# Performance work log

Hardware: AMD Instinct MI355X
Metric: run time of the kernel (lower is better)

The kernel has to match this reference:

```python
import jax, jax.numpy as jnp
import numpy as np

# Model constants (match init_kwargs)
B, V, NUM_NODES, NUM_RELS = 32, 20, 4000, 400
EMB, HID, L, N, E, OUT = 128, 128, 3, 32000, 256000, 128
DECAY = 0.03
EPS = 0.0  # self_attn eps, not trained


def setup_inputs() -> dict:
    key = jax.random.key(0)
    ks = jax.random.split(key, 20)
    s = 0.02
    return {
        "node_ids": jax.random.randint(ks[0], (N,), 0, NUM_NODES),
        "rel_ids": jax.random.randint(ks[1], (E,), 0, NUM_RELS),
        "edge_index": jax.random.randint(ks[2], (2, E), 0, N),
        "batch": jnp.sort(jax.random.randint(ks[3], (N,), 0, B)),
        "visit_node": jax.random.uniform(ks[4], (B, V, NUM_NODES), dtype=jnp.float32),
        "ehr_nodes": jax.random.uniform(ks[5], (B, NUM_NODES), dtype=jnp.float32),
        "node_emb": jax.random.normal(ks[6], (NUM_NODES, EMB), dtype=jnp.float32) * s,
        "rel_emb": jax.random.normal(ks[7], (NUM_RELS, EMB), dtype=jnp.float32) * s,
        "lin_w": jax.random.normal(ks[8], (HID, EMB), dtype=jnp.float32) * s,
        "lin_b": jnp.zeros((HID,), jnp.float32),
        "alpha_w": jax.random.normal(ks[9], (L, NUM_NODES, NUM_NODES), dtype=jnp.float32) * 0.002,
        "alpha_b": jnp.zeros((L, NUM_NODES), jnp.float32),
        "beta_w": jax.random.normal(ks[10], (L, 1, NUM_NODES), dtype=jnp.float32) * s,
        "beta_b": jnp.zeros((L, 1), jnp.float32),
        "wr_w": jax.random.normal(ks[11], (L, 1, HID), dtype=jnp.float32) * s,
        "wr_b": jnp.zeros((L, 1), jnp.float32),
        "nn_w": jax.random.normal(ks[12], (L, HID, HID), dtype=jnp.float32) * s,
        "nn_b": jnp.zeros((L, HID), jnp.float32),
        "mlp_w": jax.random.normal(ks[13], (OUT, 2 * HID), dtype=jnp.float32) * s,
        "mlp_b": jnp.zeros((OUT,), jnp.float32),
    }


def reference(node_ids, rel_ids, edge_index, batch, visit_node, ehr_nodes,
              node_emb, rel_emb, lin_w, lin_b, alpha_w, alpha_b, beta_w, beta_b,
              wr_w, wr_b, nn_w, nn_b, mlp_w, mlp_b):
    # visit decay weights lambda_j: (1, V, 1)
    lambda_j = jnp.exp(DECAY * (V - jnp.arange(V, dtype=jnp.float32))).reshape(1, V, 1)

    x = node_emb[node_ids] @ lin_w.T + lin_b          # (N, HID)
    edge_attr = rel_emb[rel_ids] @ lin_w.T + lin_b    # (E, HID)
    src, dst = edge_index[0], edge_index[1]
    nid_src = node_ids[src]
    b_src = batch[src]

    for l in range(L):
        # alpha: softmax over visit dim, (B, V, NUM_NODES)
        alpha = jax.nn.softmax(
            jnp.einsum('bvn,mn->bvm', visit_node, alpha_w[l]) + alpha_b[l], axis=1)
        # beta: (B, V, 1) with visit decay
        beta = jnp.tanh(
            jnp.einsum('bvn,on->bvo', visit_node, beta_w[l]) + beta_b[l]) * lambda_j
        attn = jnp.sum(alpha * beta, axis=1)          # (B, NUM_NODES)
        e_attn = attn[b_src, nid_src][:, None]        # (E, 1) per-edge attention

        # BiAttentionGNNConv message: relu(x_j * attn + W_R(edge_attr) * edge_attr)
        w_rel = edge_attr @ wr_w[l].T + wr_b[l]       # (E, 1)
        msg = jax.nn.relu(x[src] * e_attn + w_rel * edge_attr)
        agg = jax.ops.segment_sum(msg, dst, num_segments=N)  # scatter-add aggregate
        out = agg + (1.0 + EPS) * x                   # eps residual
        x = jax.nn.relu(out @ nn_w[l].T + nn_b[l])    # conv.nn Linear + outer relu

    # graph-level patient embedding: global mean pool over batch
    counts = jnp.maximum(
        jax.ops.segment_sum(jnp.ones((N, 1), x.dtype), batch, num_segments=B), 1.0)
    x_graph = jax.ops.segment_sum(x, batch, num_segments=B) / counts  # (B, HID)

    # node-level patient embedding: ehr multihot average of node embeddings
    x_node = (ehr_nodes @ node_emb) / jnp.sum(ehr_nodes, axis=1, keepdims=True)
    x_node = x_node @ lin_w.T + lin_b                 # (B, HID)

    logits = jnp.concatenate([x_graph, x_node], axis=1) @ mlp_w.T + mlp_b
    return logits
```

## Files before the change

### kernel.cpp

```cpp
#include <hip/hip_runtime.h>

namespace {

constexpr int kNodes = 4000;
constexpr int kRels  = 400;
constexpr int kB     = 32;
constexpr int kV     = 20;
constexpr int kN     = 32000;
constexpr int kE     = 256000;
constexpr int kH     = 128;
constexpr int kL     = 3;
constexpr int kMPad  = 4096;
constexpr int kKPad  = 4096;
constexpr int kBV    = kB * kV;
constexpr int kNB    = 32;
constexpr int kChunk = kE / kNB;
constexpr int kHalf  = 16000;

typedef __attribute__((ext_vector_type(8))) short bf16x8;
typedef __attribute__((ext_vector_type(4))) float f32x4;

__device__ inline unsigned short f2bf(float f){
  unsigned int u = __float_as_uint(f);
  u += 0x7FFFu + ((u >> 16) & 1u);
  return (unsigned short)(u >> 16);
}

__device__ inline void gload_lds16(const unsigned short* g, unsigned short* l){
  __builtin_amdgcn_global_load_lds(
      (const __attribute__((address_space(1))) unsigned int*)(g),
      (__attribute__((address_space(3))) unsigned int*)(l),
      16, 0, 0);
}


__global__ void transpose_kernel(const float* __restrict__ lin_w, const float* __restrict__ nn_w,
                                 float* __restrict__ lin_wT, float* __restrict__ nn_wT){
  int m = blockIdx.x;
  const float* in = (m == 0) ? lin_w : nn_w + (size_t)(m-1)*kH*kH;
  float* out      = (m == 0) ? lin_wT : nn_wT + (size_t)(m-1)*kH*kH;
  for (int i = threadIdx.x; i < kH*kH; i += blockDim.x){
    int r = i >> 7, c = i & (kH-1);
    out[c*kH + r] = in[i];
  }
}

__global__ __launch_bounds__(128) void proj_kernel(const float* __restrict__ node_emb,
    const float* __restrict__ rel_emb, const float* __restrict__ lin_wT,
    const float* __restrict__ lin_b, float* __restrict__ emb_lin, float* __restrict__ rel_lin){
  int row = blockIdx.x;
  const float* src; float* dst;
  if (row < kNodes){ src = node_emb + (size_t)row*kH; dst = emb_lin + (size_t)row*kH; }
  else             { src = rel_emb + (size_t)(row-kNodes)*kH; dst = rel_lin + (size_t)(row-kNodes)*kH; }
  __shared__ float rs[kH];
  int h = threadIdx.x;
  rs[h] = src[h];
  __syncthreads();
  float acc = lin_b[h];
#pragma unroll 8
  for (int k = 0; k < kH; k++) acc = fmaf(rs[k], lin_wT[k*kH + h], acc);
  dst[h] = acc;
}

__global__ void gather_x0_kernel(const int* __restrict__ node_ids,
                                 const float* __restrict__ emb_lin, float* __restrict__ x){
  int idx = blockIdx.x*256 + threadIdx.x;
  if (idx < kN*kH){
    int i = idx >> 7, c = idx & (kH-1);
    x[idx] = emb_lin[(size_t)node_ids[i]*kH + c];
  }
}

__global__ __launch_bounds__(128) void relterm_kernel(const float* __restrict__ rel_lin,
    const float* __restrict__ wr_w, const float* __restrict__ wr_b, float* __restrict__ relterm){
  int l = blockIdx.x / kRels, r = blockIdx.x % kRels;
  int t = threadIdx.x;
  float rl = rel_lin[(size_t)r*kH + t];
  __shared__ float red[kH];
  red[t] = rl * wr_w[l*kH + t];
  __syncthreads();
  for (int o = 64; o > 0; o >>= 1){
    if (t < o) red[t] += red[t+o];
    __syncthreads();
  }
  float w = red[0] + wr_b[l];
  relterm[((size_t)l*kRels + r)*kH + t] = w * rl;
}


__global__ __launch_bounds__(256) void csr_hist_kernel(const int* __restrict__ dst,
    unsigned short* __restrict__ rank, unsigned int* __restrict__ hpart){
  __shared__ unsigned int hb[kHalf];
  int p = blockIdx.x;
  int base = blockIdx.y * kHalf;
  int t = threadIdx.x;
  for (int i = t; i < kHalf; i += 256) hb[i] = 0u;
  __syncthreads();
  for (int i = t; i < kChunk; i += 256){
    int e = p*kChunk + i;
    int d = dst[e];
    int rel = d - base;
    if ((unsigned)rel < (unsigned)kHalf){
      rank[e] = (unsigned short)atomicAdd(&hb[rel], 1u);
    }
  }
  __syncthreads();
  for (int i = t; i < kHalf; i += 256)
    hpart[(size_t)p*kN + base + i] = hb[i];
}

__global__ __launch_bounds__(256) void csr_col_kernel(unsigned int* __restrict__ hpart,
    int* __restrict__ deg){
  int bin = blockIdx.x*256 + threadIdx.x;
  if (bin >= kN) return;
  unsigned int s = 0;
#pragma unroll
  for (int p = 0; p < kNB; p++){
    size_t idx = (size_t)p*kN + bin;
    unsigned int v = hpart[idx];
    hpart[idx] = s;
    s += v;
  }
  deg[bin] = (int)s;
}

__global__ __launch_bounds__(256) void scanA_kernel(const int* __restrict__ deg,
    int* __restrict__ starts, int* __restrict__ bsum){
  __shared__ int buf[256];
  int gid = blockIdx.x*256 + threadIdx.x;
  int t = threadIdx.x;
  int v = (gid < kN) ? deg[gid] : 0;
  buf[t] = v;
  __syncthreads();
  for (int o = 1; o < 256; o <<= 1){
    int add = (t >= o) ? buf[t-o] : 0;
    __syncthreads();
    buf[t] += add;
    __syncthreads();
  }
  if (gid < kN) starts[gid] = buf[t] - v;
  if (t == 255) bsum[blockIdx.x] = buf[255];
}

__global__ __launch_bounds__(128) void scanB_kernel(const int* __restrict__ bsum,
    int* __restrict__ boffs, int nblk){
  __shared__ int buf[128];
  int t = threadIdx.x;
  int v = (t < nblk) ? bsum[t] : 0;
  buf[t] = v;
  __syncthreads();
  for (int o = 1; o < 128; o <<= 1){
    int add = (t >= o) ? buf[t-o] : 0;
    __syncthreads();
    buf[t] += add;
    __syncthreads();
  }
  if (t < nblk) boffs[t] = buf[t] - v;
}

__global__ __launch_bounds__(256) void scanC_kernel(int* __restrict__ starts,
    const int* __restrict__ boffs){
  int gid = blockIdx.x*256 + threadIdx.x;
  if (gid < kN) starts[gid] += boffs[blockIdx.x];
  if (gid == kN-1) starts[kN] = kE;
}

__global__ __launch_bounds__(256) void csr_place_kernel(const int* __restrict__ dst,
    const int* __restrict__ starts, const unsigned int* __restrict__ colOff,
    const unsigned short* __restrict__ rank, int* __restrict__ perm){
  int blk = blockIdx.x;
  int p = blk >> 2;
  for (int i = threadIdx.x; i < 2000; i += 256){
    int e = blk*2000 + i;
    int d = dst[e];
    int pos = starts[d] + (int)colOff[(size_t)p*kN + d] + (int)rank[e];
    perm[pos] = e;
  }
}

__global__ void ub_kernel(const int* __restrict__ batch, int* __restrict__ ub){
  int j = threadIdx.x;
  if (j > kB) return;
  int lo = 0, hi = kN;
  while (lo < hi){
    int mid = (lo + hi) >> 1;
    if (batch[mid] < j) lo = mid + 1; else hi = mid;
  }
  ub[j] = lo;
}


__global__ void cvt_visit_kernel(const float* __restrict__ visit, unsigned short* __restrict__ out){
  int i = blockIdx.x*256 + threadIdx.x;
  if (i >= kBV*(kKPad/8)) return;
  int row = i >> 9;
  int col = (i & 511) * 8;
  unsigned short r[8];
  if (col < kNodes){
    const float* p = visit + (size_t)row*kNodes + col;
    const float4 a = *reinterpret_cast<const float4*>(p);
    const float4 b = *reinterpret_cast<const float4*>(p + 4);
    r[0]=f2bf(a.x); r[1]=f2bf(a.y); r[2]=f2bf(a.z); r[3]=f2bf(a.w);
    r[4]=f2bf(b.x); r[5]=f2bf(b.y); r[6]=f2bf(b.z); r[7]=f2bf(b.w);
  } else {
    for (int q = 0; q < 8; q++) r[q] = 0;
  }
  *reinterpret_cast<uint4*>(out + (size_t)row*kKPad + col) = *reinterpret_cast<uint4*>(r);
}

__global__ void cvtW_kernel(const float* __restrict__ W, unsigned short* __restrict__ out){
  int i = blockIdx.x*256 + threadIdx.x;
  constexpr int perL = kMPad*(kKPad/8);
  if (i >= kL*perL) return;
  int l = i / perL;
  int rem = i - l*perL;
  int row = rem >> 9;
  int col = (rem & 511) * 8;
  unsigned short r[8];
  if (row < kNodes && col < kNodes){
    const float* p = W + (size_t)l*kNodes*kNodes + (size_t)row*kNodes + col;
    const float4 a = *reinterpret_cast<const float4*>(p);
    const float4 b = *reinterpret_cast<const float4*>(p + 4);
    r[0]=f2bf(a.x); r[1]=f2bf(a.y); r[2]=f2bf(a.z); r[3]=f2bf(a.w);
    r[4]=f2bf(b.x); r[5]=f2bf(b.y); r[6]=f2bf(b.z); r[7]=f2bf(b.w);
  } else {
    for (int q = 0; q < 8; q++) r[q] = 0;
  }
  *reinterpret_cast<uint4*>(out + (size_t)l*kMPad*kKPad + (size_t)row*kKPad + col)
      = *reinterpret_cast<uint4*>(r);
}

__global__ __launch_bounds__(256) void gemm_bt_bf16(const unsigned short* __restrict__ A,
    const unsigned short* __restrict__ Ball, float* __restrict__ Sbase){
  __shared__ unsigned short As[128*64];
  __shared__ unsigned short Bs[128*64];
  int wg = (blockIdx.x & 7)*120 + (blockIdx.x >> 3);
  int lz = wg / 160;
  int rem = wg - lz*160;
  int bn = rem / 5;
  int bm = rem - bn*5;
  int l = lz >> 1, z = lz & 1;
  const unsigned short* B = Ball + (size_t)l*kMPad*kKPad;
  float* C = Sbase + (size_t)lz*kBV*kMPad;
  int kBase = z * 2048;

  int t = threadIdx.x;
  int lane = t & 63, wave = t >> 6;
  int wm = (wave >> 1) * 64, wn = (wave & 1) * 64;
  int r = lane & 15, g = lane >> 4;

  int ri = lane >> 3, s = lane & 7;
  int koff = ((s ^ ri) << 3);
  const unsigned short* Ag = A + (size_t)(bm*128 + wave*32 + ri)*kKPad + kBase + koff;
  const unsigned short* Bg = B + (size_t)(bn*128 + wave*32 + ri)*kKPad + kBase + koff;
  const size_t chunkStep = (size_t)8*kKPad;

  f32x4 acc[4][4];
#pragma unroll
  for (int i = 0; i < 4; i++)
#pragma unroll
    for (int j = 0; j < 4; j++) acc[i][j] = f32x4{0.f,0.f,0.f,0.f};

  for (int k0 = 0; k0 < 2048; k0 += 64){
    __syncthreads();
#pragma unroll
    for (int c = 0; c < 4; c++){
      gload_lds16(Ag + c*chunkStep, &As[(wave*32 + c*8)*64]);
      gload_lds16(Bg + c*chunkStep, &Bs[(wave*32 + c*8)*64]);
    }
    Ag += 64; Bg += 64;
    __syncthreads();
#pragma unroll
    for (int ksub = 0; ksub < 2; ksub++){
      bf16x8 af[4], bf[4];
#pragma unroll
      for (int i = 0; i < 4; i++){
        int arow = wm + i*16 + r;
        int brow = wn + i*16 + r;
        int slot = ((ksub << 2) + g);
        af[i] = *reinterpret_cast<const bf16x8*>(&As[arow*64 + ((slot ^ (arow & 7)) << 3)]);
        bf[i] = *reinterpret_cast<const bf16x8*>(&Bs[brow*64 + ((slot ^ (brow & 7)) << 3)]);
      }
#pragma unroll
      for (int i = 0; i < 4; i++)
#pragma unroll
        for (int j = 0; j < 4; j++)
          acc[i][j] = __builtin_amdgcn_mfma_f32_16x16x32_bf16(af[i], bf[j], acc[i][j], 0, 0, 0);
    }
  }
#pragma unroll
  for (int i = 0; i < 4; i++)
#pragma unroll
    for (int j = 0; j < 4; j++){
      int row = bm*128 + wm + i*16 + g*4;
      int col = bn*128 + wn + j*16 + r;
#pragma unroll
      for (int q = 0; q < 4; q++)
        C[(size_t)(row + q)*kMPad + col] = acc[i][j][q];
    }
}

__global__ __launch_bounds__(256) void beta_all_kernel(const float* __restrict__ visit,
    const float* __restrict__ beta_w, const float* __restrict__ beta_b,
    float* __restrict__ beta){
  int wid = (blockIdx.x*256 + threadIdx.x) >> 6;
  int lane = threadIdx.x & 63;
  if (wid >= kL*kBV) return;
  int l = wid / kBV, bv = wid - l*kBV;
  const float* row = visit + (size_t)bv*kNodes;
  const float* bw = beta_w + (size_t)l*kNodes;
  float s = 0.f;
  for (int k = lane; k < kNodes; k += 64) s = fmaf(row[k], bw[k], s);
#pragma unroll
  for (int o = 32; o > 0; o >>= 1) s += __shfl_down(s, o);
  if (lane == 0){
    int v = bv % kV;
    float lam = __expf(0.03f * (float)(kV - v));
    beta[wid] = tanhf(s + beta_b[l]) * lam;
  }
}

__global__ __launch_bounds__(256) void attn_kernel(const float* __restrict__ S,
    const float* __restrict__ beta, float* __restrict__ attn){
  int idx = blockIdx.x*256 + threadIdx.x;
  if (idx >= kL*kB*kNodes) return;
  int l = idx / (kB*kNodes);
  int rem = idx - l*(kB*kNodes);
  int b = rem / kNodes;
  int m = rem - b*kNodes;
  const float* S0 = S + (size_t)(l*2)*kBV*kMPad + (size_t)b*kV*kMPad + m;
  const float* S1 = S0 + (size_t)kBV*kMPad;
  float vals[kV];
  float mx = -1e30f;
#pragma unroll
  for (int v = 0; v < kV; v++){
    float s = S0[(size_t)v*kMPad] + S1[(size_t)v*kMPad];
    vals[v] = s; mx = fmaxf(mx, s);
  }
  float se = 0.f, ws = 0.f;
  const float* bp = beta + l*kBV + b*kV;
#pragma unroll
  for (int v = 0; v < kV; v++){ float e = __expf(vals[v] - mx); se += e; ws = fmaf(e, bp[v], ws); }
  attn[idx] = ws / se;
}

__global__ void attn_gather_kernel(const int* __restrict__ batch,
    const int* __restrict__ node_ids, const float* __restrict__ attn,
    float* __restrict__ att_n){
  int idx = blockIdx.x*256 + threadIdx.x;
  if (idx >= kL*kN) return;
  int l = idx / kN, n = idx - l*kN;
  att_n[idx] = attn[(size_t)l*kB*kNodes + (size_t)batch[n]*kNodes + node_ids[n]];
}


__global__ __launch_bounds__(256) void agg_kernel(const int* __restrict__ starts,
    const int* __restrict__ perm, const int* __restrict__ src, const int* __restrict__ rel_ids,
    const float* __restrict__ att_n_l, const float* __restrict__ relterm_l,
    const float* __restrict__ x, float* __restrict__ agg){
  int wid = (blockIdx.x*256 + threadIdx.x) >> 6;
  int lane = threadIdx.x & 63;
  if (wid >= kN) return;
  int p0 = starts[wid], p1 = starts[wid+1];
  int c = lane*2;
  float a0 = 0.f, a1 = 0.f;
  for (int p = p0; p < p1; p++){
    int e = perm[p];
    int s = src[e];
    float at = att_n_l[s];
    float2 xv = *reinterpret_cast<const float2*>(&x[(size_t)s*kH + c]);
    float2 rt = *reinterpret_cast<const float2*>(&relterm_l[(size_t)rel_ids[e]*kH + c]);
    float m0 = fmaf(xv.x, at, rt.x); m0 = m0 > 0.f ? m0 : 0.f;
    float m1 = fmaf(xv.y, at, rt.y); m1 = m1 > 0.f ? m1 : 0.f;
    a0 += m0; a1 += m1;
  }
  *reinterpret_cast<float2*>(&agg[(size_t)wid*kH + c]) = float2{a0, a1};
}

__global__ __launch_bounds__(256) void nn_kernel(const float* __restrict__ agg,
    float* __restrict__ x, const float* __restrict__ nn_wT_l, const float* __restrict__ nn_b_l){
  __shared__ float rows[8][kH];
  int rb = blockIdx.x * 8;
  int t = threadIdx.x;
#pragma unroll
  for (int i = 0; i < 4; i++){
    int idx = t + i*256;
    int rr = idx >> 7, cc = idx & (kH-1);
    size_t gi = (size_t)(rb + rr)*kH + cc;
    rows[rr][cc] = agg[gi] + x[gi];
  }
  __syncthreads();
  int cc = t & (kH-1);
  int r0 = (t >> 7) * 4;
  float acc0 = 0.f, acc1 = 0.f, acc2 = 0.f, acc3 = 0.f;
#pragma unroll 8
  for (int k = 0; k < kH; k++){
    float w = nn_wT_l[k*kH + cc];
    acc0 = fmaf(rows[r0+0][k], w, acc0);
    acc1 = fmaf(rows[r0+1][k], w, acc1);
    acc2 = fmaf(rows[r0+2][k], w, acc2);
    acc3 = fmaf(rows[r0+3][k], w, acc3);
  }
  float b = nn_b_l[cc];
  x[(size_t)(rb+r0+0)*kH + cc] = fmaxf(acc0 + b, 0.f);
  x[(size_t)(rb+r0+1)*kH + cc] = fmaxf(acc1 + b, 0.f);
  x[(size_t)(rb+r0+2)*kH + cc] = fmaxf(acc2 + b, 0.f);
  x[(size_t)(rb+r0+3)*kH + cc] = fmaxf(acc3 + b, 0.f);
}


__global__ __launch_bounds__(128) void pool_part_kernel(const float* __restrict__ x,
    const int* __restrict__ ub, float* __restrict__ pp){
  int s = blockIdx.x, b = blockIdx.y, c = threadIdx.x;
  int lo = ub[b], len = ub[b+1] - lo;
  int i0 = lo + (int)(((long long)len * s) >> 3);
  int i1 = lo + (int)(((long long)len * (s+1)) >> 3);
  float acc = 0.f;
  for (int i = i0; i < i1; i++) acc += x[(size_t)i*kH + c];
  pp[(size_t)(b*8 + s)*kH + c] = acc;
}

__global__ __launch_bounds__(128) void xnode1_kernel(const float* __restrict__ ehr,
    const float* __restrict__ node_emb, float* __restrict__ pn, float* __restrict__ ps){
  int s = blockIdx.x, b = blockIdx.y, c = threadIdx.x;
  int n0 = s * (kNodes/8), n1 = n0 + (kNodes/8);
  float acc = 0.f, es = 0.f;
  for (int n = n0; n < n1; n++){
    float e = ehr[(size_t)b*kNodes + n];
    es += e;
    acc = fmaf(e, node_emb[(size_t)n*kH + c], acc);
  }
  pn[(size_t)(b*8 + s)*kH + c] = acc;
  if (c == 0) ps[b*8 + s] = es;
}

__global__ __launch_bounds__(128) void readout_kernel(const float* __restrict__ pp,
    const int* __restrict__ ub, const float* __restrict__ pn, const float* __restrict__ ps,
    const float* __restrict__ lin_wT, const float* __restrict__ lin_b,
    const float* __restrict__ mlp_w, const float* __restrict__ mlp_b,
    float* __restrict__ out){
  int b = blockIdx.x, h = threadIdx.x;
  __shared__ float v[2*kH];
  __shared__ float ts[kH];
  float s = 0.f;
#pragma unroll
  for (int q = 0; q < 8; q++) s += pp[(size_t)(b*8 + q)*kH + h];
  int len = ub[b+1] - ub[b]; if (len < 1) len = 1;
  v[h] = s / (float)len;
  float acc = 0.f, es = 0.f;
#pragma unroll
  for (int q = 0; q < 8; q++){
    acc += pn[(size_t)(b*8 + q)*kH + h];
    es  += ps[b*8 + q];
  }
  ts[h] = acc / es;
  __syncthreads();
  float r = lin_b[h];
#pragma unroll 8
  for (int k = 0; k < kH; k++) r = fmaf(ts[k], lin_wT[k*kH + h], r);
  v[kH + h] = r;
  __syncthreads();
  float o = mlp_b[h];
#pragma unroll 8
  for (int k = 0; k < 2*kH; k++) o = fmaf(v[k], mlp_w[(size_t)h*2*kH + k], o);
  out[b*kH + h] = o;
}

}

extern "C" void kernel_launch(void* const* d_in, const int* in_sizes, int n_in,
                              void* d_out, int out_size, void* d_ws, size_t ws_size,
                              hipStream_t stream){
  const int*   node_ids = (const int*)d_in[0];
  const int*   rel_ids  = (const int*)d_in[1];
  const int*   e_src    = (const int*)d_in[2];
  const int*   e_dst    = e_src + kE;
  const int*   batch    = (const int*)d_in[3];
  const float* visit    = (const float*)d_in[4];
  const float* ehr      = (const float*)d_in[5];
  const float* node_emb = (const float*)d_in[6];
  const float* rel_emb  = (const float*)d_in[7];
  const float* lin_w    = (const float*)d_in[8];
  const float* lin_b    = (const float*)d_in[9];
  const float* alpha_w  = (const float*)d_in[10];
  const float* beta_w   = (const float*)d_in[12];
  const float* beta_b   = (const float*)d_in[13];
  const float* wr_w     = (const float*)d_in[14];
  const float* wr_b     = (const float*)d_in[15];
  const float* nn_w     = (const float*)d_in[16];
  const float* nn_b     = (const float*)d_in[17];
  const float* mlp_w    = (const float*)d_in[18];
  const float* mlp_b    = (const float*)d_in[19];
  float* out = (float*)d_out;

  char* w = (char*)d_ws;
  auto alloc = [&](size_t bytes)->char*{
    char* p = w; w += (bytes + 255) & ~(size_t)255; return p;
  };
  int*   starts = (int*)  alloc((size_t)(kN+1)*4);
  int*   deg    = (int*)  alloc((size_t)kN*4);
  int*   bsum   = (int*)  alloc(256*4);
  int*   boffs  = (int*)  alloc(256*4);
  int*   ub     = (int*)  alloc((kB+1)*4);
  int*   perm   = (int*)  alloc((size_t)kE*4);
  unsigned short* rank = (unsigned short*)alloc((size_t)kE*2);
  unsigned int* hpart  = (unsigned int*)alloc((size_t)kNB*kN*4);
  float* embLin = (float*)alloc((size_t)kNodes*kH*4);
  float* relLin = (float*)alloc((size_t)kRels*kH*4);
  float* relterm= (float*)alloc((size_t)kL*kRels*kH*4);
  float* linwT  = (float*)alloc((size_t)kH*kH*4);
  float* nnwT   = (float*)alloc((size_t)kL*kH*kH*4);
  float* x      = (float*)alloc((size_t)kN*kH*4);
  float* agg    = (float*)alloc((size_t)kN*kH*4);
  unsigned short* visitbf = (unsigned short*)alloc((size_t)kBV*kKPad*2);
  unsigned short* awbf    = (unsigned short*)alloc((size_t)kL*kMPad*kKPad*2);
  float* S      = (float*)alloc((size_t)kL*2*kBV*kMPad*4);
  float* attn   = (float*)alloc((size_t)kL*kB*kNodes*4);
  float* att_n  = (float*)alloc((size_t)kL*kN*4);
  float* beta   = (float*)alloc((size_t)kL*kBV*4);
  float* pp     = (float*)alloc((size_t)kB*8*kH*4);
  float* pn     = (float*)alloc((size_t)kB*8*kH*4);
  float* ps     = (float*)alloc((size_t)kB*8*4);
  if ((size_t)(w - (char*)d_ws) > ws_size) return;

  transpose_kernel<<<4, 256, 0, stream>>>(lin_w, nn_w, linwT, nnwT);
  proj_kernel<<<kNodes + kRels, 128, 0, stream>>>(node_emb, rel_emb, linwT, lin_b, embLin, relLin);
  gather_x0_kernel<<<(kN*kH)/256, 256, 0, stream>>>(node_ids, embLin, x);
  relterm_kernel<<<kL*kRels, 128, 0, stream>>>(relLin, wr_w, wr_b, relterm);

  csr_hist_kernel<<<dim3(kNB, 2), 256, 0, stream>>>(e_dst, rank, hpart);
  csr_col_kernel<<<(kN+255)/256, 256, 0, stream>>>(hpart, deg);
  scanA_kernel<<<(kN+255)/256, 256, 0, stream>>>(deg, starts, bsum);
  scanB_kernel<<<1, 128, 0, stream>>>(bsum, boffs, (kN+255)/256);
  scanC_kernel<<<(kN+255)/256, 256, 0, stream>>>(starts, boffs);
  csr_place_kernel<<<128, 256, 0, stream>>>(e_dst, starts, hpart, rank, perm);
  ub_kernel<<<1, 64, 0, stream>>>(batch, ub);

  cvt_visit_kernel<<<(kBV*(kKPad/8) + 255)/256, 256, 0, stream>>>(visit, visitbf);
  beta_all_kernel<<<kL*kBV/4, 256, 0, stream>>>(visit, beta_w, beta_b, beta);
  cvtW_kernel<<<(kL*kMPad*(kKPad/8) + 255)/256, 256, 0, stream>>>(alpha_w, awbf);
  gemm_bt_bf16<<<960, 256, 0, stream>>>(visitbf, awbf, S);
  attn_kernel<<<(kL*kB*kNodes + 255)/256, 256, 0, stream>>>(S, beta, attn);
  attn_gather_kernel<<<(kL*kN + 255)/256, 256, 0, stream>>>(batch, node_ids, attn, att_n);

  for (int l = 0; l < kL; l++){
    agg_kernel<<<kN/4, 256, 0, stream>>>(starts, perm, e_src, rel_ids,
        att_n + (size_t)l*kN, relterm + (size_t)l*kRels*kH, x, agg);
    nn_kernel<<<kN/8, 256, 0, stream>>>(agg, x, nnwT + (size_t)l*kH*kH, nn_b + (size_t)l*kH);
  }

  pool_part_kernel<<<dim3(8, kB), 128, 0, stream>>>(x, ub, pp);
  xnode1_kernel<<<dim3(8, kB), 128, 0, stream>>>(ehr, node_emb, pn, ps);
  readout_kernel<<<kB, 128, 0, stream>>>(pp, ub, pn, ps, linwT, lin_b, mlp_w, mlp_b, out);
}
```

Before: 610.7 us.

## Double-buffer GEMM LDS, drop split-K, and gather bf16 node features in aggregation

The alpha GEMM moves from split-K (two halves summed later in attn_kernel) to a full-K loop over 480 workgroups, with a double-buffered LDS staging that prefetches the next K tile while MFMAs run on the current one. The S buffer shrinks by half and attn_kernel reads one partial instead of two. Separately, a bf16 copy of x is written alongside fp32 x, and the edge aggregation gathers the bf16 copy to halve random-access traffic. The costs are reduced precision on messages, fewer workgroups for the GEMM, doubled LDS per block, and extra bf16 writes.

```diff
diff --git a/kernel.cpp b/kernel.cpp
--- a/kernel.cpp
+++ b/kernel.cpp
@@ -63,11 +63,14 @@
 }
 
 __global__ void gather_x0_kernel(const int* __restrict__ node_ids,
-                                 const float* __restrict__ emb_lin, float* __restrict__ x){
+                                 const float* __restrict__ emb_lin, float* __restrict__ x,
+                                 unsigned short* __restrict__ xbf){
   int idx = blockIdx.x*256 + threadIdx.x;
   if (idx < kN*kH){
     int i = idx >> 7, c = idx & (kH-1);
-    x[idx] = emb_lin[(size_t)node_ids[i]*kH + c];
+    float v = emb_lin[(size_t)node_ids[i]*kH + c];
+    x[idx] = v;
+    xbf[idx] = f2bf(v);
   }
 }
 
@@ -232,17 +235,15 @@
 
 __global__ __launch_bounds__(256) void gemm_bt_bf16(const unsigned short* __restrict__ A,
     const unsigned short* __restrict__ Ball, float* __restrict__ Sbase){
-  __shared__ unsigned short As[128*64];
-  __shared__ unsigned short Bs[128*64];
-  int wg = (blockIdx.x & 7)*120 + (blockIdx.x >> 3);
-  int lz = wg / 160;
-  int rem = wg - lz*160;
+  __shared__ unsigned short As[2][128*64];
+  __shared__ unsigned short Bs[2][128*64];
+  int wg = (blockIdx.x & 7)*60 + (blockIdx.x >> 3);
+  int l = wg / 160;
+  int rem = wg - l*160;
   int bn = rem / 5;
   int bm = rem - bn*5;
-  int l = lz >> 1, z = lz & 1;
   const unsigned short* B = Ball + (size_t)l*kMPad*kKPad;
-  float* C = Sbase + (size_t)lz*kBV*kMPad;
-  int kBase = z * 2048;
+  float* C = Sbase + (size_t)l*kBV*kMPad;
 
   int t = threadIdx.x;
   int lane = t & 63, wave = t >> 6;
@@ -251,25 +252,32 @@
 
   int ri = lane >> 3, s = lane & 7;
   int koff = ((s ^ ri) << 3);
-  const unsigned short* Ag = A + (size_t)(bm*128 + wave*32 + ri)*kKPad + kBase + koff;
-  const unsigned short* Bg = B + (size_t)(bn*128 + wave*32 + ri)*kKPad + kBase + koff;
+  const unsigned short* Ag = A + (size_t)(bm*128 + wave*32 + ri)*kKPad + koff;
+  const unsigned short* Bg = B + (size_t)(bn*128 + wave*32 + ri)*kKPad + koff;
   const size_t chunkStep = (size_t)8*kKPad;
 
+  auto STAGE = [&](int buf, int tstep){
+    const unsigned short* a = Ag + tstep*64;
+    const unsigned short* b = Bg + tstep*64;
+#pragma unroll
+    for (int c = 0; c < 4; c++){
+      gload_lds16(a + c*chunkStep, &As[buf][(wave*32 + c*8)*64]);
+      gload_lds16(b + c*chunkStep, &Bs[buf][(wave*32 + c*8)*64]);
+    }
+  };
+
   f32x4 acc[4][4];
 #pragma unroll
   for (int i = 0; i < 4; i++)
 #pragma unroll
     for (int j = 0; j < 4; j++) acc[i][j] = f32x4{0.f,0.f,0.f,0.f};
 
-  for (int k0 = 0; k0 < 2048; k0 += 64){
-    __syncthreads();
-#pragma unroll
-    for (int c = 0; c < 4; c++){
-      gload_lds16(Ag + c*chunkStep, &As[(wave*32 + c*8)*64]);
-      gload_lds16(Bg + c*chunkStep, &Bs[(wave*32 + c*8)*64]);
-    }
-    Ag += 64; Bg += 64;
-    __syncthreads();
+  constexpr int NT = kKPad / 64;
+  STAGE(0, 0);
+  __syncthreads();
+  int cur = 0;
+  for (int tstep = 0; tstep < NT; tstep++){
+    if (tstep + 1 < NT) STAGE(cur ^ 1, tstep + 1);
 #pragma unroll
     for (int ksub = 0; ksub < 2; ksub++){
       bf16x8 af[4], bf[4];
@@ -278,8 +286,8 @@
         int arow = wm + i*16 + r;
         int brow = wn + i*16 + r;
         int slot = ((ksub << 2) + g);
-        af[i] = *reinterpret_cast<const bf16x8*>(&As[arow*64 + ((slot ^ (arow & 7)) << 3)]);
-        bf[i] = *reinterpret_cast<const bf16x8*>(&Bs[brow*64 + ((slot ^ (brow & 7)) << 3)]);
+        af[i] = *reinterpret_cast<const bf16x8*>(&As[cur][arow*64 + ((slot ^ (arow & 7)) << 3)]);
+        bf[i] = *reinterpret_cast<const bf16x8*>(&Bs[cur][brow*64 + ((slot ^ (brow & 7)) << 3)]);
       }
 #pragma unroll
       for (int i = 0; i < 4; i++)
@@ -287,6 +295,8 @@
         for (int j = 0; j < 4; j++)
           acc[i][j] = __builtin_amdgcn_mfma_f32_16x16x32_bf16(af[i], bf[j], acc[i][j], 0, 0, 0);
     }
+    __syncthreads();
+    cur ^= 1;
   }
 #pragma unroll
   for (int i = 0; i < 4; i++)
@@ -328,13 +338,12 @@
   int rem = idx - l*(kB*kNodes);
   int b = rem / kNodes;
   int m = rem - b*kNodes;
-  const float* S0 = S + (size_t)(l*2)*kBV*kMPad + (size_t)b*kV*kMPad + m;
-  const float* S1 = S0 + (size_t)kBV*kMPad;
+  const float* S0 = S + (size_t)l*kBV*kMPad + (size_t)b*kV*kMPad + m;
   float vals[kV];
   float mx = -1e30f;
 #pragma unroll
   for (int v = 0; v < kV; v++){
-    float s = S0[(size_t)v*kMPad] + S1[(size_t)v*kMPad];
+    float s = S0[(size_t)v*kMPad];
     vals[v] = s; mx = fmaxf(mx, s);
   }
   float se = 0.f, ws = 0.f;
@@ -357,7 +366,7 @@
 __global__ __launch_bounds__(256) void agg_kernel(const int* __restrict__ starts,
     const int* __restrict__ perm, const int* __restrict__ src, const int* __restrict__ rel_ids,
     const float* __restrict__ att_n_l, const float* __restrict__ relterm_l,
-    const float* __restrict__ x, float* __restrict__ agg){
+    const unsigned short* __restrict__ xbf, float* __restrict__ agg){
   int wid = (blockIdx.x*256 + threadIdx.x) >> 6;
   int lane = threadIdx.x & 63;
   if (wid >= kN) return;
@@ -368,17 +377,20 @@
     int e = perm[p];
     int s = src[e];
     float at = att_n_l[s];
-    float2 xv = *reinterpret_cast<const float2*>(&x[(size_t)s*kH + c]);
+    unsigned int xv = *reinterpret_cast<const unsigned int*>(&xbf[(size_t)s*kH + c]);
     float2 rt = *reinterpret_cast<const float2*>(&relterm_l[(size_t)rel_ids[e]*kH + c]);
-    float m0 = fmaf(xv.x, at, rt.x); m0 = m0 > 0.f ? m0 : 0.f;
-    float m1 = fmaf(xv.y, at, rt.y); m1 = m1 > 0.f ? m1 : 0.f;
+    float x0 = __uint_as_float(xv << 16);
+    float x1 = __uint_as_float(xv & 0xFFFF0000u);
+    float m0 = fmaf(x0, at, rt.x); m0 = m0 > 0.f ? m0 : 0.f;
+    float m1 = fmaf(x1, at, rt.y); m1 = m1 > 0.f ? m1 : 0.f;
     a0 += m0; a1 += m1;
   }
   *reinterpret_cast<float2*>(&agg[(size_t)wid*kH + c]) = float2{a0, a1};
 }
 
 __global__ __launch_bounds__(256) void nn_kernel(const float* __restrict__ agg,
-    float* __restrict__ x, const float* __restrict__ nn_wT_l, const float* __restrict__ nn_b_l){
+    float* __restrict__ x, unsigned short* __restrict__ xbf,
+    const float* __restrict__ nn_wT_l, const float* __restrict__ nn_b_l){
   __shared__ float rows[8][kH];
   int rb = blockIdx.x * 8;
   int t = threadIdx.x;
@@ -402,10 +414,14 @@
     acc3 = fmaf(rows[r0+3][k], w, acc3);
   }
   float b = nn_b_l[cc];
-  x[(size_t)(rb+r0+0)*kH + cc] = fmaxf(acc0 + b, 0.f);
-  x[(size_t)(rb+r0+1)*kH + cc] = fmaxf(acc1 + b, 0.f);
-  x[(size_t)(rb+r0+2)*kH + cc] = fmaxf(acc2 + b, 0.f);
-  x[(size_t)(rb+r0+3)*kH + cc] = fmaxf(acc3 + b, 0.f);
+  float o0 = fmaxf(acc0 + b, 0.f);
+  float o1 = fmaxf(acc1 + b, 0.f);
+  float o2 = fmaxf(acc2 + b, 0.f);
+  float o3 = fmaxf(acc3 + b, 0.f);
+  x[(size_t)(rb+r0+0)*kH + cc] = o0;  xbf[(size_t)(rb+r0+0)*kH + cc] = f2bf(o0);
+  x[(size_t)(rb+r0+1)*kH + cc] = o1;  xbf[(size_t)(rb+r0+1)*kH + cc] = f2bf(o1);
+  x[(size_t)(rb+r0+2)*kH + cc] = o2;  xbf[(size_t)(rb+r0+2)*kH + cc] = f2bf(o2);
+  x[(size_t)(rb+r0+3)*kH + cc] = o3;  xbf[(size_t)(rb+r0+3)*kH + cc] = f2bf(o3);
 }
 
 
@@ -511,10 +527,11 @@
   float* linwT  = (float*)alloc((size_t)kH*kH*4);
   float* nnwT   = (float*)alloc((size_t)kL*kH*kH*4);
   float* x      = (float*)alloc((size_t)kN*kH*4);
+  unsigned short* xbf = (unsigned short*)alloc((size_t)kN*kH*2);
   float* agg    = (float*)alloc((size_t)kN*kH*4);
   unsigned short* visitbf = (unsigned short*)alloc((size_t)kBV*kKPad*2);
   unsigned short* awbf    = (unsigned short*)alloc((size_t)kL*kMPad*kKPad*2);
-  float* S      = (float*)alloc((size_t)kL*2*kBV*kMPad*4);
+  float* S      = (float*)alloc((size_t)kL*kBV*kMPad*4);
   float* attn   = (float*)alloc((size_t)kL*kB*kNodes*4);
   float* att_n  = (float*)alloc((size_t)kL*kN*4);
   float* beta   = (float*)alloc((size_t)kL*kBV*4);
@@ -525,7 +542,7 @@
 
   transpose_kernel<<<4, 256, 0, stream>>>(lin_w, nn_w, linwT, nnwT);
   proj_kernel<<<kNodes + kRels, 128, 0, stream>>>(node_emb, rel_emb, linwT, lin_b, embLin, relLin);
-  gather_x0_kernel<<<(kN*kH)/256, 256, 0, stream>>>(node_ids, embLin, x);
+  gather_x0_kernel<<<(kN*kH)/256, 256, 0, stream>>>(node_ids, embLin, x, xbf);
   relterm_kernel<<<kL*kRels, 128, 0, stream>>>(relLin, wr_w, wr_b, relterm);
 
   csr_hist_kernel<<<dim3(kNB, 2), 256, 0, stream>>>(e_dst, rank, hpart);
@@ -539,14 +556,14 @@
   cvt_visit_kernel<<<(kBV*(kKPad/8) + 255)/256, 256, 0, stream>>>(visit, visitbf);
   beta_all_kernel<<<kL*kBV/4, 256, 0, stream>>>(visit, beta_w, beta_b, beta);
   cvtW_kernel<<<(kL*kMPad*(kKPad/8) + 255)/256, 256, 0, stream>>>(alpha_w, awbf);
-  gemm_bt_bf16<<<960, 256, 0, stream>>>(visitbf, awbf, S);
+  gemm_bt_bf16<<<480, 256, 0, stream>>>(visitbf, awbf, S);
   attn_kernel<<<(kL*kB*kNodes + 255)/256, 256, 0, stream>>>(S, beta, attn);
   attn_gather_kernel<<<(kL*kN + 255)/256, 256, 0, stream>>>(batch, node_ids, attn, att_n);
 
   for (int l = 0; l < kL; l++){
     agg_kernel<<<kN/4, 256, 0, stream>>>(starts, perm, e_src, rel_ids,
-        att_n + (size_t)l*kN, relterm + (size_t)l*kRels*kH, x, agg);
-    nn_kernel<<<kN/8, 256, 0, stream>>>(agg, x, nnwT + (size_t)l*kH*kH, nn_b + (size_t)l*kH);
+        att_n + (size_t)l*kN, relterm + (size_t)l*kRels*kH, xbf, agg);
+    nn_kernel<<<kN/8, 256, 0, stream>>>(agg, x, xbf, nnwT + (size_t)l*kH*kH, nn_b + (size_t)l*kH);
   }
 
   pool_part_kernel<<<dim3(8, kB), 128, 0, stream>>>(x, ub, pp);
```

After: 598.3 us. -2.0%, faster.

## Fuse aggregation with NN layer, bf16 features, pre-permuted edges, unpadded double-buffered GEMM

Applied to the files above, without the earlier changes.

Merges the per-layer aggregation and the dense NN update into one kernel, removing the agg buffer round-trip and one launch per layer. The CSR placement now writes permuted src and rel arrays directly, and per-edge attention is precomputed, so each edge needs one fewer indirection. Neighbour features are gathered from a bf16 copy of x to halve gather traffic. The attention GEMM drops its K padding from 4096 to 4000 and uses double-buffered 32-wide K tiles so loads overlap compute. The bf16 message inputs lower precision, and the extra per-edge attention array adds memory traffic.

```diff
diff --git a/kernel.cpp b/kernel.cpp
--- a/kernel.cpp
+++ b/kernel.cpp
@@ -11,7 +11,7 @@
 constexpr int kH     = 128;
 constexpr int kL     = 3;
 constexpr int kMPad  = 4096;
-constexpr int kKPad  = 4096;
+constexpr int kKW    = 4000;
 constexpr int kBV    = kB * kV;
 constexpr int kNB    = 32;
 constexpr int kChunk = kE / kNB;
@@ -63,11 +63,14 @@
 }
 
 __global__ void gather_x0_kernel(const int* __restrict__ node_ids,
-                                 const float* __restrict__ emb_lin, float* __restrict__ x){
+                                 const float* __restrict__ emb_lin, float* __restrict__ x,
+                                 unsigned short* __restrict__ xbf){
   int idx = blockIdx.x*256 + threadIdx.x;
   if (idx < kN*kH){
     int i = idx >> 7, c = idx & (kH-1);
-    x[idx] = emb_lin[(size_t)node_ids[i]*kH + c];
+    float v = emb_lin[(size_t)node_ids[i]*kH + c];
+    x[idx] = v;
+    xbf[idx] = f2bf(v);
   }
 }
 
@@ -166,15 +169,18 @@
 }
 
 __global__ __launch_bounds__(256) void csr_place_kernel(const int* __restrict__ dst,
+    const int* __restrict__ src, const int* __restrict__ rel_ids,
     const int* __restrict__ starts, const unsigned int* __restrict__ colOff,
-    const unsigned short* __restrict__ rank, int* __restrict__ perm){
+    const unsigned short* __restrict__ rank,
+    int* __restrict__ src_perm, int* __restrict__ rel_perm){
   int blk = blockIdx.x;
   int p = blk >> 2;
   for (int i = threadIdx.x; i < 2000; i += 256){
     int e = blk*2000 + i;
     int d = dst[e];
     int pos = starts[d] + (int)colOff[(size_t)p*kN + d] + (int)rank[e];
-    perm[pos] = e;
+    src_perm[pos] = src[e];
+    rel_perm[pos] = rel_ids[e];
   }
 }
 
@@ -192,12 +198,28 @@
 
 __global__ void cvt_visit_kernel(const float* __restrict__ visit, unsigned short* __restrict__ out){
   int i = blockIdx.x*256 + threadIdx.x;
-  if (i >= kBV*(kKPad/8)) return;
-  int row = i >> 9;
-  int col = (i & 511) * 8;
+  if (i >= kBV*(kKW/8)) return;
+  int row = i / (kKW/8);
+  int col = (i - row*(kKW/8)) * 8;
+  const float* p = visit + (size_t)row*kKW + col;
+  const float4 a = *reinterpret_cast<const float4*>(p);
+  const float4 b = *reinterpret_cast<const float4*>(p + 4);
+  unsigned short r[8] = {f2bf(a.x),f2bf(a.y),f2bf(a.z),f2bf(a.w),
+                         f2bf(b.x),f2bf(b.y),f2bf(b.z),f2bf(b.w)};
+  *reinterpret_cast<uint4*>(out + (size_t)row*kKW + col) = *reinterpret_cast<uint4*>(r);
+}
+
+__global__ void cvtW_kernel(const float* __restrict__ W, unsigned short* __restrict__ out){
+  int i = blockIdx.x*256 + threadIdx.x;
+  constexpr int perL = kMPad*(kKW/8);
+  if (i >= kL*perL) return;
+  int l = i / perL;
+  int rem = i - l*perL;
+  int row = rem / (kKW/8);
+  int col = (rem - row*(kKW/8)) * 8;
   unsigned short r[8];
-  if (col < kNodes){
-    const float* p = visit + (size_t)row*kNodes + col;
+  if (row < kNodes){
+    const float* p = W + (size_t)l*kNodes*kNodes + (size_t)row*kKW + col;
     const float4 a = *reinterpret_cast<const float4*>(p);
     const float4 b = *reinterpret_cast<const float4*>(p + 4);
     r[0]=f2bf(a.x); r[1]=f2bf(a.y); r[2]=f2bf(a.z); r[3]=f2bf(a.w);
@@ -205,55 +227,35 @@
   } else {
     for (int q = 0; q < 8; q++) r[q] = 0;
   }
-  *reinterpret_cast<uint4*>(out + (size_t)row*kKPad + col) = *reinterpret_cast<uint4*>(r);
-}
-
-__global__ void cvtW_kernel(const float* __restrict__ W, unsigned short* __restrict__ out){
-  int i = blockIdx.x*256 + threadIdx.x;
-  constexpr int perL = kMPad*(kKPad/8);
-  if (i >= kL*perL) return;
-  int l = i / perL;
-  int rem = i - l*perL;
-  int row = rem >> 9;
-  int col = (rem & 511) * 8;
-  unsigned short r[8];
-  if (row < kNodes && col < kNodes){
-    const float* p = W + (size_t)l*kNodes*kNodes + (size_t)row*kNodes + col;
-    const float4 a = *reinterpret_cast<const float4*>(p);
-    const float4 b = *reinterpret_cast<const float4*>(p + 4);
-    r[0]=f2bf(a.x); r[1]=f2bf(a.y); r[2]=f2bf(a.z); r[3]=f2bf(a.w);
-    r[4]=f2bf(b.x); r[5]=f2bf(b.y); r[6]=f2bf(b.z); r[7]=f2bf(b.w);
-  } else {
-    for (int q = 0; q < 8; q++) r[q] = 0;
-  }
-  *reinterpret_cast<uint4*>(out + (size_t)l*kMPad*kKPad + (size_t)row*kKPad + col)
+  *reinterpret_cast<uint4*>(out + (size_t)l*kMPad*kKW + (size_t)row*kKW + col)
       = *reinterpret_cast<uint4*>(r);
 }
 
 __global__ __launch_bounds__(256) void gemm_bt_bf16(const unsigned short* __restrict__ A,
     const unsigned short* __restrict__ Ball, float* __restrict__ Sbase){
-  __shared__ unsigned short As[128*64];
-  __shared__ unsigned short Bs[128*64];
+  __shared__ unsigned short As[2][128*32];
+  __shared__ unsigned short Bs[2][128*32];
   int wg = (blockIdx.x & 7)*120 + (blockIdx.x >> 3);
   int lz = wg / 160;
   int rem = wg - lz*160;
   int bn = rem / 5;
   int bm = rem - bn*5;
   int l = lz >> 1, z = lz & 1;
-  const unsigned short* B = Ball + (size_t)l*kMPad*kKPad;
+  const unsigned short* B = Ball + (size_t)l*kMPad*kKW;
   float* C = Sbase + (size_t)lz*kBV*kMPad;
-  int kBase = z * 2048;
+  int tile0 = z ? 63 : 0;
+  int nt    = z ? 62 : 63;
 
   int t = threadIdx.x;
   int lane = t & 63, wave = t >> 6;
   int wm = (wave >> 1) * 64, wn = (wave & 1) * 64;
   int r = lane & 15, g = lane >> 4;
 
-  int ri = lane >> 3, s = lane & 7;
-  int koff = ((s ^ ri) << 3);
-  const unsigned short* Ag = A + (size_t)(bm*128 + wave*32 + ri)*kKPad + kBase + koff;
-  const unsigned short* Bg = B + (size_t)(bn*128 + wave*32 + ri)*kKPad + kBase + koff;
-  const size_t chunkStep = (size_t)8*kKPad;
+  int ri = lane >> 2, s = lane & 3;
+  int koff = ((s ^ ((ri >> 1) & 3)) << 3);
+  const unsigned short* Ag = A + (size_t)(bm*128 + wave*32 + ri)*kKW + tile0*32 + koff;
+  const unsigned short* Bg = B + (size_t)(bn*128 + wave*32 + ri)*kKW + tile0*32 + koff;
+  const size_t rstep = (size_t)16*kKW;
 
   f32x4 acc[4][4];
 #pragma unroll
@@ -261,32 +263,35 @@
 #pragma unroll
     for (int j = 0; j < 4; j++) acc[i][j] = f32x4{0.f,0.f,0.f,0.f};
 
-  for (int k0 = 0; k0 < 2048; k0 += 64){
+  auto STAGE = [&](int buf, int ts){
+    const unsigned short* a = Ag + ts*32;
+    const unsigned short* b = Bg + ts*32;
+    gload_lds16(a,         &As[buf][(wave*32     )*32]);
+    gload_lds16(a + rstep, &As[buf][(wave*32 + 16)*32]);
+    gload_lds16(b,         &Bs[buf][(wave*32     )*32]);
+    gload_lds16(b + rstep, &Bs[buf][(wave*32 + 16)*32]);
+  };
+
+  STAGE(0, 0);
+  for (int ts = 0; ts < nt; ts++){
+    int cur = ts & 1;
     __syncthreads();
-#pragma unroll
-    for (int c = 0; c < 4; c++){
-      gload_lds16(Ag + c*chunkStep, &As[(wave*32 + c*8)*64]);
-      gload_lds16(Bg + c*chunkStep, &Bs[(wave*32 + c*8)*64]);
+    if (ts + 1 < nt) STAGE(cur ^ 1, ts + 1);
+    bf16x8 af[4], bf[4];
+#pragma unroll
+    for (int i = 0; i < 4; i++){
+      int arow = wm + i*16 + r;
+      int brow = wn + i*16 + r;
+      af[i] = *reinterpret_cast<const bf16x8*>(
+          &As[cur][arow*32 + ((g ^ ((arow >> 1) & 3)) << 3)]);
+      bf[i] = *reinterpret_cast<const bf16x8*>(
+          &Bs[cur][brow*32 + ((g ^ ((brow >> 1) & 3)) << 3)]);
     }
-    Ag += 64; Bg += 64;
-    __syncthreads();
-#pragma unroll
-    for (int ksub = 0; ksub < 2; ksub++){
-      bf16x8 af[4], bf[4];
-#pragma unroll
-      for (int i = 0; i < 4; i++){
-        int arow = wm + i*16 + r;
-        int brow = wn + i*16 + r;
-        int slot = ((ksub << 2) + g);
-        af[i] = *reinterpret_cast<const bf16x8*>(&As[arow*64 + ((slot ^ (arow & 7)) << 3)]);
-        bf[i] = *reinterpret_cast<const bf16x8*>(&Bs[brow*64 + ((slot ^ (brow & 7)) << 3)]);
-      }
-#pragma unroll
-      for (int i = 0; i < 4; i++)
-#pragma unroll
-        for (int j = 0; j < 4; j++)
-          acc[i][j] = __builtin_amdgcn_mfma_f32_16x16x32_bf16(af[i], bf[j], acc[i][j], 0, 0, 0);
-    }
+#pragma unroll
+    for (int i = 0; i < 4; i++)
+#pragma unroll
+      for (int j = 0; j < 4; j++)
+        acc[i][j] = __builtin_amdgcn_mfma_f32_16x16x32_bf16(af[i], bf[j], acc[i][j], 0, 0, 0);
   }
 #pragma unroll
   for (int i = 0; i < 4; i++)
@@ -344,68 +349,60 @@
   attn[idx] = ws / se;
 }
 
-__global__ void attn_gather_kernel(const int* __restrict__ batch,
+__global__ void att_e_kernel(const int* __restrict__ src_perm, const int* __restrict__ batch,
     const int* __restrict__ node_ids, const float* __restrict__ attn,
-    float* __restrict__ att_n){
+    float* __restrict__ att_e){
   int idx = blockIdx.x*256 + threadIdx.x;
-  if (idx >= kL*kN) return;
-  int l = idx / kN, n = idx - l*kN;
-  att_n[idx] = attn[(size_t)l*kB*kNodes + (size_t)batch[n]*kNodes + node_ids[n]];
-}
-
-
-__global__ __launch_bounds__(256) void agg_kernel(const int* __restrict__ starts,
-    const int* __restrict__ perm, const int* __restrict__ src, const int* __restrict__ rel_ids,
-    const float* __restrict__ att_n_l, const float* __restrict__ relterm_l,
-    const float* __restrict__ x, float* __restrict__ agg){
-  int wid = (blockIdx.x*256 + threadIdx.x) >> 6;
-  int lane = threadIdx.x & 63;
-  if (wid >= kN) return;
-  int p0 = starts[wid], p1 = starts[wid+1];
+  if (idx >= kL*kE) return;
+  int l = idx / kE, p = idx - l*kE;
+  int s = src_perm[p];
+  att_e[idx] = attn[(size_t)l*kB*kNodes + (size_t)batch[s]*kNodes + node_ids[s]];
+}
+
+
+__global__ __launch_bounds__(512) void aggnn_kernel(const int* __restrict__ starts,
+    const int* __restrict__ src_perm, const int* __restrict__ rel_perm,
+    const float* __restrict__ att_e_l, const float* __restrict__ relterm_l,
+    const unsigned short* __restrict__ xbf_in, unsigned short* __restrict__ xbf_out,
+    float* __restrict__ x, const float* __restrict__ nn_wT_l, const float* __restrict__ nn_b_l){
+  __shared__ float rows[8][kH];
+  int t = threadIdx.x;
+  int wv = t >> 6, lane = t & 63;
+  int node = blockIdx.x*8 + wv;
+  int p0 = starts[node], p1 = starts[node+1];
   int c = lane*2;
   float a0 = 0.f, a1 = 0.f;
   for (int p = p0; p < p1; p++){
-    int e = perm[p];
-    int s = src[e];
-    float at = att_n_l[s];
-    float2 xv = *reinterpret_cast<const float2*>(&x[(size_t)s*kH + c]);
-    float2 rt = *reinterpret_cast<const float2*>(&relterm_l[(size_t)rel_ids[e]*kH + c]);
-    float m0 = fmaf(xv.x, at, rt.x); m0 = m0 > 0.f ? m0 : 0.f;
-    float m1 = fmaf(xv.y, at, rt.y); m1 = m1 > 0.f ? m1 : 0.f;
+    float at = att_e_l[p];
+    int s = src_perm[p];
+    int rel = rel_perm[p];
+    unsigned int xv = *reinterpret_cast<const unsigned int*>(&xbf_in[(size_t)s*kH + c]);
+    float2 rt = *reinterpret_cast<const float2*>(&relterm_l[(size_t)rel*kH + c]);
+    float x0 = __uint_as_float(xv << 16);
+    float x1 = __uint_as_float(xv & 0xFFFF0000u);
+    float m0 = fmaf(x0, at, rt.x); m0 = m0 > 0.f ? m0 : 0.f;
+    float m1 = fmaf(x1, at, rt.y); m1 = m1 > 0.f ? m1 : 0.f;
     a0 += m0; a1 += m1;
   }
-  *reinterpret_cast<float2*>(&agg[(size_t)wid*kH + c]) = float2{a0, a1};
-}
-
-__global__ __launch_bounds__(256) void nn_kernel(const float* __restrict__ agg,
-    float* __restrict__ x, const float* __restrict__ nn_wT_l, const float* __restrict__ nn_b_l){
-  __shared__ float rows[8][kH];
-  int rb = blockIdx.x * 8;
-  int t = threadIdx.x;
-#pragma unroll
-  for (int i = 0; i < 4; i++){
-    int idx = t + i*256;
-    int rr = idx >> 7, cc = idx & (kH-1);
-    size_t gi = (size_t)(rb + rr)*kH + cc;
-    rows[rr][cc] = agg[gi] + x[gi];
-  }
-  __syncthreads();
-  int cc = t & (kH-1);
-  int r0 = (t >> 7) * 4;
-  float acc0 = 0.f, acc1 = 0.f, acc2 = 0.f, acc3 = 0.f;
+  size_t gi = (size_t)node*kH + c;
+  rows[wv][c]   = a0 + x[gi];
+  rows[wv][c+1] = a1 + x[gi+1];
+  __syncthreads();
+  int cc = t & 127;
+  int r0 = (t >> 7) * 2;
+  float acc0 = 0.f, acc1 = 0.f;
 #pragma unroll 8
   for (int k = 0; k < kH; k++){
     float w = nn_wT_l[k*kH + cc];
-    acc0 = fmaf(rows[r0+0][k], w, acc0);
+    acc0 = fmaf(rows[r0  ][k], w, acc0);
     acc1 = fmaf(rows[r0+1][k], w, acc1);
-    acc2 = fmaf(rows[r0+2][k], w, acc2);
-    acc3 = fmaf(rows[r0+3][k], w, acc3);
   }
   float b = nn_b_l[cc];
-  x[(size_t)(rb+r0+0)*kH + cc] = fmaxf(acc0 + b, 0.f);
-  x[(size_t)(rb+r0+1)*kH + cc] = fmaxf(acc1 + b, 0.f);
-  x[(size_t)(rb+r0+2)*kH + cc] = fmaxf(acc2 + b, 0.f);
-  x[(size_t)(rb+r0+3)*kH + cc] = fmaxf(acc3 + b, 0.f);
+  float o0 = fmaxf(acc0 + b, 0.f);
+  float o1 = fmaxf(acc1 + b, 0.f);
+  size_t n0 = (size_t)(blockIdx.x*8 + r0)*kH + cc;
+  x[n0]        = o0;  xbf_out[n0]        = f2bf(o0);
+  x[n0 + kH]   = o1;  xbf_out[n0 + kH]   = f2bf(o1);
 }
 
 
@@ -502,7 +499,8 @@
   int*   bsum   = (int*)  alloc(256*4);
   int*   boffs  = (int*)  alloc(256*4);
   int*   ub     = (int*)  alloc((kB+1)*4);
-  int*   perm   = (int*)  alloc((size_t)kE*4);
+  int*   src_perm = (int*)alloc((size_t)kE*4);
+  int*   rel_perm = (int*)alloc((size_t)kE*4);
   unsigned short* rank = (unsigned short*)alloc((size_t)kE*2);
   unsigned int* hpart  = (unsigned int*)alloc((size_t)kNB*kN*4);
   float* embLin = (float*)alloc((size_t)kNodes*kH*4);
@@ -511,12 +509,13 @@
   float* linwT  = (float*)alloc((size_t)kH*kH*4);
   float* nnwT   = (float*)alloc((size_t)kL*kH*kH*4);
   float* x      = (float*)alloc((size_t)kN*kH*4);
-  float* agg    = (float*)alloc((size_t)kN*kH*4);
-  unsigned short* visitbf = (unsigned short*)alloc((size_t)kBV*kKPad*2);
-  unsigned short* awbf    = (unsigned short*)alloc((size_t)kL*kMPad*kKPad*2);
+  unsigned short* xbfA = (unsigned short*)alloc((size_t)kN*kH*2);
+  unsigned short* xbfB = (unsigned short*)alloc((size_t)kN*kH*2);
+  unsigned short* visitbf = (unsigned short*)alloc((size_t)kBV*kKW*2);
+  unsigned short* awbf    = (unsigned short*)alloc((size_t)kL*kMPad*kKW*2);
   float* S      = (float*)alloc((size_t)kL*2*kBV*kMPad*4);
   float* attn   = (float*)alloc((size_t)kL*kB*kNodes*4);
-  float* att_n  = (float*)alloc((size_t)kL*kN*4);
+  float* att_e  = (float*)alloc((size_t)kL*kE*4);
   float* beta   = (float*)alloc((size_t)kL*kBV*4);
   float* pp     = (float*)alloc((size_t)kB*8*kH*4);
   float* pn     = (float*)alloc((size_t)kB*8*kH*4);
@@ -525,7 +524,7 @@
 
   transpose_kernel<<<4, 256, 0, stream>>>(lin_w, nn_w, linwT, nnwT);
   proj_kernel<<<kNodes + kRels, 128, 0, stream>>>(node_emb, rel_emb, linwT, lin_b, embLin, relLin);
-  gather_x0_kernel<<<(kN*kH)/256, 256, 0, stream>>>(node_ids, embLin, x);
+  gather_x0_kernel<<<(kN*kH)/256, 256, 0, stream>>>(node_ids, embLin, x, xbfA);
   relterm_kernel<<<kL*kRels, 128, 0, stream>>>(relLin, wr_w, wr_b, relterm);
 
   csr_hist_kernel<<<dim3(kNB, 2), 256, 0, stream>>>(e_dst, rank, hpart);
@@ -533,20 +532,24 @@
   scanA_kernel<<<(kN+255)/256, 256, 0, stream>>>(deg, starts, bsum);
   scanB_kernel<<<1, 128, 0, stream>>>(bsum, boffs, (kN+255)/256);
   scanC_kernel<<<(kN+255)/256, 256, 0, stream>>>(starts, boffs);
-  csr_place_kernel<<<128, 256, 0, stream>>>(e_dst, starts, hpart, rank, perm);
+  csr_place_kernel<<<128, 256, 0, stream>>>(e_dst, e_src, rel_ids, starts, hpart, rank,
+                                            src_perm, rel_perm);
   ub_kernel<<<1, 64, 0, stream>>>(batch, ub);
 
-  cvt_visit_kernel<<<(kBV*(kKPad/8) + 255)/256, 256, 0, stream>>>(visit, visitbf);
+  cvt_visit_kernel<<<(kBV*(kKW/8) + 255)/256, 256, 0, stream>>>(visit, visitbf);
   beta_all_kernel<<<kL*kBV/4, 256, 0, stream>>>(visit, beta_w, beta_b, beta);
-  cvtW_kernel<<<(kL*kMPad*(kKPad/8) + 255)/256, 256, 0, stream>>>(alpha_w, awbf);
+  cvtW_kernel<<<(kL*kMPad*(kKW/8) + 255)/256, 256, 0, stream>>>(alpha_w, awbf);
   gemm_bt_bf16<<<960, 256, 0, stream>>>(visitbf, awbf, S);
   attn_kernel<<<(kL*kB*kNodes + 255)/256, 256, 0, stream>>>(S, beta, attn);
-  attn_gather_kernel<<<(kL*kN + 255)/256, 256, 0, stream>>>(batch, node_ids, attn, att_n);
-
+  att_e_kernel<<<(kL*kE + 255)/256, 256, 0, stream>>>(src_perm, batch, node_ids, attn, att_e);
+
+  unsigned short* xin = xbfA;
+  unsigned short* xout = xbfB;
   for (int l = 0; l < kL; l++){
-    agg_kernel<<<kN/4, 256, 0, stream>>>(starts, perm, e_src, rel_ids,
-        att_n + (size_t)l*kN, relterm + (size_t)l*kRels*kH, x, agg);
-    nn_kernel<<<kN/8, 256, 0, stream>>>(agg, x, nnwT + (size_t)l*kH*kH, nn_b + (size_t)l*kH);
+    aggnn_kernel<<<kN/8, 512, 0, stream>>>(starts, src_perm, rel_perm,
+        att_e + (size_t)l*kE, relterm + (size_t)l*kRels*kH,
+        xin, xout, x, nnwT + (size_t)l*kH*kH, nn_b + (size_t)l*kH);
+    unsigned short* tmp = xin; xin = xout; xout = tmp;
   }
 
   pool_part_kernel<<<dim3(8, kB), 128, 0, stream>>>(x, ub, pp);
```

New measurement: 593.4 us. 2.8% less time.
